# Kernel optimization log

Measured on AMD Instinct MI355X. Metric: run time of the kernel, lower is better.

Reference implementation:

```python
import jax, jax.numpy as jnp
import numpy as np

IN_FEATURES = 8192
OUT_FEATURES = 14336
M_TOKENS = 64


def _dequant_rowwise_int4(w_packed, w_scales):
    # w_packed: [out, in//2], each byte holds two signed int4 values
    # (low nibble = even k index, high nibble = odd k index, two's complement)
    low = w_packed & 0xF
    high = (w_packed >> 4) & 0xF
    q = jnp.stack([low, high], axis=-1).reshape(w_packed.shape[0], -1)  # [out, in]
    q = jnp.where(q >= 8, q - 16, q).astype(jnp.float32)
    return q * w_scales[:, None]  # [out, in]


def setup_inputs() -> dict:
    key = jax.random.key(0)
    k1, k2, k3, k4 = jax.random.split(key, 4)
    x = jax.random.normal(k1, (M_TOKENS, IN_FEATURES), dtype=jnp.float32)
    w_packed = jax.random.randint(k2, (OUT_FEATURES, IN_FEATURES // 2), 0, 256, dtype=jnp.int32)
    # per-row scales, small positive values as produced by max-abs/7 quantization
    w_scales = jax.random.uniform(k3, (OUT_FEATURES,), dtype=jnp.float32) * 0.02 + 1e-4
    bias = jax.random.normal(k4, (OUT_FEATURES,), dtype=jnp.float32)
    return {"x": x, "w_packed": w_packed, "w_scales": w_scales, "bias": bias}


def reference(x, w_packed, w_scales, bias):
    original_shape = x.shape[:-1]
    x_2d = x.reshape(-1, IN_FEATURES)
    w = _dequant_rowwise_int4(w_packed, w_scales)  # [out, in]
    y = x_2d @ w.T + bias[None, :]  # [M, out]
    return y.reshape(*original_shape, OUT_FEATURES)
```

## Files before the change

### kernel.cpp

```cpp
#include <hip/hip_runtime.h>

#define IN_F   8192
#define OUT_F  14336
#define M_TOK  64
#define KP     (IN_F / 2)
#define BN     64
#define KSPLIT 4
#define KCHUNK (IN_F / KSPLIT)
#define NBLK   (OUT_F / BN)

typedef __attribute__((ext_vector_type(8))) short bf16x8;
typedef __attribute__((ext_vector_type(4))) float f32x4;

__device__ __forceinline__ unsigned short f2bf_rne(float f) {
    unsigned u = __builtin_bit_cast(unsigned, f);
    u += 0x7FFFu + ((u >> 16) & 1u);
    return (unsigned short)(u >> 16);
}

__global__ __launch_bounds__(256) void qlin_prep(const float* __restrict__ x,
                                                 const float* __restrict__ bias,
                                                 unsigned short* __restrict__ xb,
                                                 float* __restrict__ out) {
    const int XV = (M_TOK * IN_F) / 4;
    const int OV = (M_TOK * OUT_F) / 4;
    int gid = blockIdx.x * 256 + threadIdx.x;
    if (gid < XV) {
        float4 v = reinterpret_cast<const float4*>(x)[gid];
        ushort4 o;
        o.x = f2bf_rne(v.x);
        o.y = f2bf_rne(v.y);
        o.z = f2bf_rne(v.z);
        o.w = f2bf_rne(v.w);
        reinterpret_cast<ushort4*>(xb)[gid] = o;
    } else {
        int og = gid - XV;
        if (og < OV) {
            float4 b = reinterpret_cast<const float4*>(bias)[og % (OUT_F / 4)];
            reinterpret_cast<float4*>(out)[og] = b;
        }
    }
}

__device__ __forceinline__ int unpack2_bf16(int v) {
    int q0 = ((int)((unsigned)v << 28)) >> 28;
    int q1 = ((int)((unsigned)v << 24)) >> 28;
    float f0 = (float)q0;
    float f1 = (float)q1;
    unsigned u0 = __builtin_bit_cast(unsigned, f0);
    unsigned u1 = __builtin_bit_cast(unsigned, f1);
    return (int)((u0 >> 16) | (u1 & 0xFFFF0000u));
}

__global__ __launch_bounds__(256) void qlin_gemm(const unsigned short* __restrict__ xb,
                                                 const int* __restrict__ wp,
                                                 const float* __restrict__ scales,
                                                 float* __restrict__ out) {
    const int wave = threadIdx.x >> 6;
    const int lane = threadIdx.x & 63;
    const int t = lane & 15;
    const int q = lane >> 4;

    const int nblk = blockIdx.x % NBLK;
    const int kblk = blockIdx.x / NBLK;

    const int n  = nblk * BN + wave * 16 + t;
    const int k0 = kblk * KCHUNK + q * 8;

    const int*            __restrict__ wptr = wp + n * KP + (k0 >> 1);
    const unsigned short* __restrict__ xptr = xb + t * IN_F + k0;

    f32x4 acc0 = {0.f, 0.f, 0.f, 0.f};
    f32x4 acc1 = acc0, acc2 = acc0, acc3 = acc0;

#pragma unroll 4
    for (int kk = 0; kk < KCHUNK; kk += 32) {
        int4 wv = *reinterpret_cast<const int4*>(wptr + (kk >> 1));
        bf16x8 a0 = *reinterpret_cast<const bf16x8*>(xptr + kk);
        bf16x8 a1 = *reinterpret_cast<const bf16x8*>(xptr + 16 * IN_F + kk);
        bf16x8 a2 = *reinterpret_cast<const bf16x8*>(xptr + 32 * IN_F + kk);
        bf16x8 a3 = *reinterpret_cast<const bf16x8*>(xptr + 48 * IN_F + kk);

        int4 pk;
        pk.x = unpack2_bf16(wv.x);
        pk.y = unpack2_bf16(wv.y);
        pk.z = unpack2_bf16(wv.z);
        pk.w = unpack2_bf16(wv.w);
        bf16x8 b = __builtin_bit_cast(bf16x8, pk);

        acc0 = __builtin_amdgcn_mfma_f32_16x16x32_bf16(a0, b, acc0, 0, 0, 0);
        acc1 = __builtin_amdgcn_mfma_f32_16x16x32_bf16(a1, b, acc1, 0, 0, 0);
        acc2 = __builtin_amdgcn_mfma_f32_16x16x32_bf16(a2, b, acc2, 0, 0, 0);
        acc3 = __builtin_amdgcn_mfma_f32_16x16x32_bf16(a3, b, acc3, 0, 0, 0);
    }

    const float sc = scales[n];
    const int mrow = q * 4;
#pragma unroll
    for (int r = 0; r < 4; ++r) {
        atomicAdd(&out[(     mrow + r) * OUT_F + n], acc0[r] * sc);
        atomicAdd(&out[(16 + mrow + r) * OUT_F + n], acc1[r] * sc);
        atomicAdd(&out[(32 + mrow + r) * OUT_F + n], acc2[r] * sc);
        atomicAdd(&out[(48 + mrow + r) * OUT_F + n], acc3[r] * sc);
    }
}

extern "C" void kernel_launch(void* const* d_in, const int* in_sizes, int n_in,
                              void* d_out, int out_size, void* d_ws, size_t ws_size,
                              hipStream_t stream) {
    const float* x     = (const float*)d_in[0];
    const int*   wp    = (const int*)d_in[1];
    const float* sc    = (const float*)d_in[2];
    const float* bias  = (const float*)d_in[3];
    float* out = (float*)d_out;
    unsigned short* xb = (unsigned short*)d_ws;

    const int prep_items = (M_TOK * IN_F) / 4 + (M_TOK * OUT_F) / 4;
    qlin_prep<<<(prep_items + 255) / 256, 256, 0, stream>>>(x, bias, xb, out);
    qlin_gemm<<<NBLK * KSPLIT, 256, 0, stream>>>(xb, wp, sc, out);
}
```

Measured before the change: 409.9 us.

## Stage weight and activation tiles through LDS and switch to 32x32 MFMA

Replaces direct per-lane global loads with cooperative global_load_lds staging of 128x128 weight tiles and 64x128 activation tiles, then computes with 32x32x16 bf16 MFMA. Tile width and K split are doubled, keeping the same block count. This aims to issue more memory requests in flight per step and reuse loaded activations across more output columns. It adds two barriers per step with no double buffering, and may suffer LDS bank conflicts from the power-of-two row strides.

After: 358.2 us. 1.14x faster.

```diff
diff --git a/kernel.cpp b/kernel.cpp
--- a/kernel.cpp
+++ b/kernel.cpp
@@ -3,14 +3,16 @@
 #define IN_F   8192
 #define OUT_F  14336
 #define M_TOK  64
-#define KP     (IN_F / 2)
-#define BN     64
-#define KSPLIT 4
+#define KPI    4096
+#define BN     128
+#define NBLK   (OUT_F / BN)
+#define KSPLIT 8
 #define KCHUNK (IN_F / KSPLIT)
-#define NBLK   (OUT_F / BN)
+#define BK     128
+#define NSTEP  (KCHUNK / BK)
 
-typedef __attribute__((ext_vector_type(8))) short bf16x8;
-typedef __attribute__((ext_vector_type(4))) float f32x4;
+typedef __attribute__((ext_vector_type(8)))  short bf16x8;
+typedef __attribute__((ext_vector_type(16))) float f32x16;
 
 __device__ __forceinline__ unsigned short f2bf_rne(float f) {
     unsigned u = __builtin_bit_cast(unsigned, f);
@@ -45,73 +47,99 @@
 __device__ __forceinline__ int unpack2_bf16(int v) {
     int q0 = ((int)((unsigned)v << 28)) >> 28;
     int q1 = ((int)((unsigned)v << 24)) >> 28;
-    float f0 = (float)q0;
-    float f1 = (float)q1;
-    unsigned u0 = __builtin_bit_cast(unsigned, f0);
-    unsigned u1 = __builtin_bit_cast(unsigned, f1);
+    unsigned u0 = __builtin_bit_cast(unsigned, (float)q0);
+    unsigned u1 = __builtin_bit_cast(unsigned, (float)q1);
     return (int)((u0 >> 16) | (u1 & 0xFFFF0000u));
+}
+
+__device__ __forceinline__ bf16x8 unpack_b(int4 wv) {
+    int4 pk;
+    pk.x = unpack2_bf16(wv.x);
+    pk.y = unpack2_bf16(wv.y);
+    pk.z = unpack2_bf16(wv.z);
+    pk.w = unpack2_bf16(wv.w);
+    return __builtin_bit_cast(bf16x8, pk);
+}
+
+__device__ __forceinline__ void gload_lds16(const void* g, void* l) {
+    __builtin_amdgcn_global_load_lds(
+        (const __attribute__((address_space(1))) unsigned int*)g,
+        (__attribute__((address_space(3))) unsigned int*)l,
+        16, 0, 0);
 }
 
 __global__ __launch_bounds__(256) void qlin_gemm(const unsigned short* __restrict__ xb,
                                                  const int* __restrict__ wp,
                                                  const float* __restrict__ scales,
                                                  float* __restrict__ out) {
-    const int wave = threadIdx.x >> 6;
-    const int lane = threadIdx.x & 63;
-    const int t = lane & 15;
-    const int q = lane >> 4;
+    __shared__ int            wlds[BN * (BK / 2)];
+    __shared__ unsigned short xlds[M_TOK * BK];
+
+    const int tid  = threadIdx.x;
+    const int wave = tid >> 6;
+    const int lane = tid & 63;
+    const int tp   = lane & 31;
+    const int qp   = lane >> 5;
 
     const int nblk = blockIdx.x % NBLK;
     const int kblk = blockIdx.x / NBLK;
+    const int n0   = nblk * BN;
+    const int kb   = kblk * KCHUNK;
 
-    const int n  = nblk * BN + wave * 16 + t;
-    const int k0 = kblk * KCHUNK + q * 8;
+    f32x16 acc0 = {0.f,0.f,0.f,0.f,0.f,0.f,0.f,0.f,0.f,0.f,0.f,0.f,0.f,0.f,0.f,0.f};
+    f32x16 acc1 = acc0;
 
-    const int*            __restrict__ wptr = wp + n * KP + (k0 >> 1);
-    const unsigned short* __restrict__ xptr = xb + t * IN_F + k0;
+    for (int step = 0; step < NSTEP; ++step) {
+#pragma unroll
+        for (int j = 0; j < 8; ++j) {
+            int li = (wave * 8 + j) * 64 + lane;
+            int r  = li >> 4;
+            int c  = li & 15;
+            const int* gp = wp + (size_t)(n0 + r) * KPI + (kb >> 1) + step * (BK / 2) + c * 4;
+            gload_lds16(gp, (char*)wlds + (size_t)li * 16);
+        }
+#pragma unroll
+        for (int j = 0; j < 4; ++j) {
+            int li = (wave * 4 + j) * 64 + lane;
+            int r  = li >> 4;
+            int c  = li & 15;
+            const unsigned short* gp = xb + (size_t)r * IN_F + kb + step * BK + c * 8;
+            gload_lds16(gp, (char*)xlds + (size_t)li * 16);
+        }
+        __syncthreads();
 
-    f32x4 acc0 = {0.f, 0.f, 0.f, 0.f};
-    f32x4 acc1 = acc0, acc2 = acc0, acc3 = acc0;
-
-#pragma unroll 4
-    for (int kk = 0; kk < KCHUNK; kk += 32) {
-        int4 wv = *reinterpret_cast<const int4*>(wptr + (kk >> 1));
-        bf16x8 a0 = *reinterpret_cast<const bf16x8*>(xptr + kk);
-        bf16x8 a1 = *reinterpret_cast<const bf16x8*>(xptr + 16 * IN_F + kk);
-        bf16x8 a2 = *reinterpret_cast<const bf16x8*>(xptr + 32 * IN_F + kk);
-        bf16x8 a3 = *reinterpret_cast<const bf16x8*>(xptr + 48 * IN_F + kk);
-
-        int4 pk;
-        pk.x = unpack2_bf16(wv.x);
-        pk.y = unpack2_bf16(wv.y);
-        pk.z = unpack2_bf16(wv.z);
-        pk.w = unpack2_bf16(wv.w);
-        bf16x8 b = __builtin_bit_cast(bf16x8, pk);
-
-        acc0 = __builtin_amdgcn_mfma_f32_16x16x32_bf16(a0, b, acc0, 0, 0, 0);
-        acc1 = __builtin_amdgcn_mfma_f32_16x16x32_bf16(a1, b, acc1, 0, 0, 0);
-        acc2 = __builtin_amdgcn_mfma_f32_16x16x32_bf16(a2, b, acc2, 0, 0, 0);
-        acc3 = __builtin_amdgcn_mfma_f32_16x16x32_bf16(a3, b, acc3, 0, 0, 0);
+#pragma unroll
+        for (int kf = 0; kf < 8; ++kf) {
+            int4 wv = *reinterpret_cast<const int4*>(
+                (const char*)wlds + ((wave * 32 + tp) * (BK / 2) + kf * 8 + qp * 4) * 4);
+            bf16x8 b  = unpack_b(wv);
+            bf16x8 a0 = *reinterpret_cast<const bf16x8*>(
+                (const char*)xlds + ((tp)      * BK + kf * 16 + qp * 8) * 2);
+            bf16x8 a1 = *reinterpret_cast<const bf16x8*>(
+                (const char*)xlds + ((32 + tp) * BK + kf * 16 + qp * 8) * 2);
+            acc0 = __builtin_amdgcn_mfma_f32_32x32x16_bf16(a0, b, acc0, 0, 0, 0);
+            acc1 = __builtin_amdgcn_mfma_f32_32x32x16_bf16(a1, b, acc1, 0, 0, 0);
+        }
+        __syncthreads();
     }
 
+    const int   n  = n0 + wave * 32 + tp;
     const float sc = scales[n];
-    const int mrow = q * 4;
 #pragma unroll
-    for (int r = 0; r < 4; ++r) {
-        atomicAdd(&out[(     mrow + r) * OUT_F + n], acc0[r] * sc);
-        atomicAdd(&out[(16 + mrow + r) * OUT_F + n], acc1[r] * sc);
-        atomicAdd(&out[(32 + mrow + r) * OUT_F + n], acc2[r] * sc);
-        atomicAdd(&out[(48 + mrow + r) * OUT_F + n], acc3[r] * sc);
+    for (int reg = 0; reg < 16; ++reg) {
+        int m = (reg & 3) + 8 * (reg >> 2) + 4 * qp;
+        atomicAdd(&out[(size_t)m        * OUT_F + n], acc0[reg] * sc);
+        atomicAdd(&out[(size_t)(32 + m) * OUT_F + n], acc1[reg] * sc);
     }
 }
 
 extern "C" void kernel_launch(void* const* d_in, const int* in_sizes, int n_in,
                               void* d_out, int out_size, void* d_ws, size_t ws_size,
                               hipStream_t stream) {
-    const float* x     = (const float*)d_in[0];
-    const int*   wp    = (const int*)d_in[1];
-    const float* sc    = (const float*)d_in[2];
-    const float* bias  = (const float*)d_in[3];
+    const float* x    = (const float*)d_in[0];
+    const int*   wp   = (const int*)d_in[1];
+    const float* sc   = (const float*)d_in[2];
+    const float* bias = (const float*)d_in[3];
     float* out = (float*)d_out;
     unsigned short* xb = (unsigned short*)d_ws;
 
```
